# Optimization experiments

Hardware: AMD Instinct MI355X
Metric: run time of the kernel (lower is better)

The kernel has to match this reference:

```python
import jax, jax.numpy as jnp
import numpy as np

C, H, K, G = 256, 8, 32, 8
HD = C // H
SCALE = HD ** -0.5
POS_BND = int(0.8 * K * 1 ** 0.5)  # 25
RPE_NUM = 2 * POS_BND + 1          # 51
NW = 4096


def setup_inputs() -> dict:
    key = jax.random.key(0)
    ks = jax.random.split(key, 8)
    data = jax.random.normal(ks[0], (NW * (K + G), C), dtype=jnp.float32)
    # relative xyz offsets between points in a window; exercise the clamp
    rel_pos = jax.random.randint(ks[1], (NW, K, K, 3), -POS_BND - 5, POS_BND + 6).astype(jnp.int32)
    # additive mask: 0 for valid pairs, -100 for masked (padded) pairs
    keep = jax.random.bernoulli(ks[2], 0.9, (NW, K + G, K + G))
    mask = jnp.where(keep, 0.0, -100.0).astype(jnp.float32)
    qkv_w = jax.random.normal(ks[3], (C, 3 * C), dtype=jnp.float32) * (C ** -0.5)
    qkv_b = jnp.zeros((3 * C,), dtype=jnp.float32)
    proj_w = jax.random.normal(ks[4], (C, C), dtype=jnp.float32) * (C ** -0.5)
    proj_b = jnp.zeros((C,), dtype=jnp.float32)
    rpe_table = jax.random.normal(ks[5], (3 * RPE_NUM, H), dtype=jnp.float32) * 0.02
    return {"data": data, "rel_pos": rel_pos, "mask": mask, "qkv_w": qkv_w,
            "qkv_b": qkv_b, "proj_w": proj_w, "proj_b": proj_b, "rpe_table": rpe_table}


def reference(data, rel_pos, mask, qkv_w, qkv_b, proj_w, proj_b, rpe_table):
    W = K + G  # window size including context tokens
    qkv = data @ qkv_w + qkv_b                              # (T, 3C)
    qkv_std = jnp.std(qkv, axis=0, ddof=1)                  # torch .std is unbiased
    qkv = qkv.reshape(-1, W, 3, H, HD).transpose(2, 0, 3, 1, 4)  # (3, Nw, H, W, HD)
    q, k, v = qkv[0] * SCALE, qkv[1], qkv[2]
    attn = jnp.einsum('nhqd,nhkd->nhqk', q, k)              # (Nw, H, W, W)
    # RPE: clamp offsets, index per-axis slices of table, sum over xyz
    idx = jnp.clip(rel_pos, -POS_BND, POS_BND) + POS_BND + jnp.arange(3, dtype=rel_pos.dtype) * RPE_NUM
    rpe = rpe_table[idx].sum(axis=3)                        # (Nw, K, K, H)
    rpe = rpe.transpose(0, 3, 1, 2)                         # (Nw, H, K, K)
    rpe = jnp.pad(rpe, ((0, 0), (0, 0), (G, 0), (G, 0)))    # pad for context tokens
    attn = attn + rpe + mask[:, None]
    attn = jax.nn.softmax(attn, axis=-1)
    out = jnp.einsum('nhqk,nhkd->nqhd', attn, v).reshape(-1, W, C)
    out = out @ proj_w + proj_b                             # (Nw, W, C)
    return (out, qkv_std)
```

## Files before the change

### kernel.cpp

```cpp
#include <hip/hip_runtime.h>
#include <math.h>

#define SCALE_F 0.17677669529663687f

typedef __bf16 bf16x8 __attribute__((ext_vector_type(8)));
typedef float f32x4 __attribute__((ext_vector_type(4)));

__device__ __forceinline__ unsigned short f2bf(float f) {
  unsigned u = __builtin_bit_cast(unsigned, f);
  u = (u + 0x7FFFu + ((u >> 16) & 1u)) >> 16;
  return (unsigned short)u;
}
__device__ __forceinline__ float bf2f(unsigned short u) {
  return __builtin_bit_cast(float, (unsigned)u << 16);
}
__device__ __forceinline__ unsigned pk2(float a, float b) {
  return (unsigned)f2bf(a) | ((unsigned)f2bf(b) << 16);
}
__device__ __forceinline__ bf16x8 ld16(const void* p) {
  int4 v = *(const int4*)p;
  return __builtin_bit_cast(bf16x8, v);
}
__device__ __forceinline__ void gll16(const void* g, void* l) {
  __builtin_amdgcn_global_load_lds(
      (const __attribute__((address_space(1))) unsigned int*)g,
      (__attribute__((address_space(3))) unsigned int*)l, 16, 0, 0);
}


__global__ void octa_prep2(const float* __restrict__ qkv_w, const float* __restrict__ proj_w,
                           unsigned short* __restrict__ wTq, unsigned short* __restrict__ pTq)
{
  int e = blockIdx.x * 256 + threadIdx.x;
  if (e < 196608) {
    int c = e >> 13;
    int nc = c >> 3, kc = c & 7;
    int p2 = e & 8191;
    int n = p2 >> 5, cw = p2 & 31;
    int kl = cw ^ (((n >> 1) & 3) << 3);
    wTq[e] = f2bf(qkv_w[(size_t)(kc * 32 + kl) * 768 + nc * 256 + n]);
  } else {
    int e2 = e - 196608;
    int kc = e2 >> 13, p2 = e2 & 8191;
    int n = p2 >> 5, cw = p2 & 31;
    int kl = cw ^ (((n >> 1) & 3) << 3);
    pTq[e2] = f2bf(proj_w[(size_t)(kc * 32 + kl) * 256 + n]);
  }
}

__global__ __launch_bounds__(256)
void octa_bias(const float* __restrict__ maskp, const int* __restrict__ rel_pos,
               const float* __restrict__ rpe_table, char* __restrict__ biasg)
{
  __shared__ char bl[25600];
  const int w = blockIdx.x, tid = threadIdx.x;
  for (int e = tid; e < 1600; e += 256) {
    int qi = e / 40, kj = e - qi * 40;
    float m = maskp[(size_t)w * 1600 + qi * 40 + kj];
    float b8[8];
    if (qi >= 8 && kj >= 8) {
      const int* rp = rel_pos + ((size_t)w * 1024 + (qi - 8) * 32 + (kj - 8)) * 3;
      int c0 = rp[0], c1 = rp[1], c2 = rp[2];
      c0 = min(25, max(-25, c0)); c1 = min(25, max(-25, c1)); c2 = min(25, max(-25, c2));
      const float4* r0 = (const float4*)(rpe_table + (c0 + 25) * 8);
      const float4* r1 = (const float4*)(rpe_table + (c1 + 76) * 8);
      const float4* r2 = (const float4*)(rpe_table + (c2 + 127) * 8);
      float4 a0 = r0[0], a1 = r1[0], a2 = r2[0];
      float4 b0 = r0[1], b1 = r1[1], b2 = r2[1];
      b8[0] = m + a0.x + a1.x + a2.x; b8[1] = m + a0.y + a1.y + a2.y;
      b8[2] = m + a0.z + a1.z + a2.z; b8[3] = m + a0.w + a1.w + a2.w;
      b8[4] = m + b0.x + b1.x + b2.x; b8[5] = m + b0.y + b1.y + b2.y;
      b8[6] = m + b0.z + b1.z + b2.z; b8[7] = m + b0.w + b1.w + b2.w;
    } else {
      #pragma unroll
      for (int h = 0; h < 8; ++h) b8[h] = m;
    }
    #pragma unroll
    for (int h = 0; h < 8; ++h)
      *(unsigned short*)(bl + h * 3200 + kj * 80 + qi * 2) = f2bf(b8[h]);
  }
  __syncthreads();
  for (int f = tid; f < 1600; f += 256)
    *(int4*)(biasg + (size_t)w * 40960 + f * 16) = *(const int4*)(bl + f * 16);
}

#define KQ_A0 0
#define KQ_A1 8192
#define KQ_B0 16384
#define KQ_B1 32768
#define KQ_LDS 49152

__global__ __launch_bounds__(512, 4)
void octa_qkv(const float* __restrict__ data, const float* __restrict__ qkv_b,
              const unsigned short* __restrict__ wTq, float* __restrict__ ws,
              char* __restrict__ qg, char* __restrict__ kg, char* __restrict__ vg)
{
  extern __shared__ char smem[];
  const int tid = threadIdx.x, lane = tid & 63, wid = tid >> 6;
  const int ql = lane & 15, lg = lane >> 4;
  const int bm = blockIdx.x / 3, nc = blockIdx.x - bm * 3;
  const int wr = wid >> 2, wc = wid & 3;
  const char* wbase = (const char*)wTq + (size_t)nc * 131072;

  const int arow = tid >> 2, aq = tid & 3;
  const float* abase = data + ((size_t)bm * 128 + arow) * 256 + aq * 8;
  const int alds = arow * 64 + ((aq * 16) ^ (((arow >> 1) & 3) << 4));

  float4 a0 = *(const float4*)abase;
  float4 a1 = *(const float4*)(abase + 4);
  gll16(wbase + wid * 1024 + lane * 16, smem + KQ_B0 + wid * 1024);
  gll16(wbase + 8192 + wid * 1024 + lane * 16, smem + KQ_B0 + 8192 + wid * 1024);
  *(uint2*)(smem + KQ_A0 + alds) = make_uint2(pk2(a0.x, a0.y), pk2(a0.z, a0.w));
  *(uint2*)(smem + KQ_A0 + alds + 8) = make_uint2(pk2(a1.x, a1.y), pk2(a1.z, a1.w));
  __syncthreads();

  f32x4 acc[4][4];
  #pragma unroll
  for (int m = 0; m < 4; ++m)
    #pragma unroll
    for (int n = 0; n < 4; ++n) acc[m][n] = (f32x4){0.f, 0.f, 0.f, 0.f};

  #pragma unroll
  for (int t = 0; t < 8; ++t) {
    float4 na0, na1;
    if (t < 7) {
      na0 = *(const float4*)(abase + (t + 1) * 32);
      na1 = *(const float4*)(abase + (t + 1) * 32 + 4);
      const char* bsrc = wbase + (size_t)(t + 1) * 16384;
      char* bb1 = smem + (((t + 1) & 1) ? KQ_B1 : KQ_B0);
      gll16(bsrc + wid * 1024 + lane * 16, bb1 + wid * 1024);
      gll16(bsrc + 8192 + wid * 1024 + lane * 16, bb1 + 8192 + wid * 1024);
    }
    const char* ab = smem + ((t & 1) ? KQ_A1 : KQ_A0);
    const char* bb = smem + ((t & 1) ? KQ_B1 : KQ_B0);
    bf16x8 af[4], bf[4];
    #pragma unroll
    for (int mt = 0; mt < 4; ++mt) {
      int row = wr * 64 + mt * 16 + ql;
      af[mt] = ld16(ab + row * 64 + ((lg * 16) ^ (((row >> 1) & 3) << 4)));
    }
    #pragma unroll
    for (int nt = 0; nt < 4; ++nt) {
      int n = wc * 64 + nt * 16 + ql;
      bf[nt] = ld16(bb + n * 64 + ((lg * 16) ^ (((n >> 1) & 3) << 4)));
    }
    #pragma unroll
    for (int nt = 0; nt < 4; ++nt)
      #pragma unroll
      for (int mt = 0; mt < 4; ++mt)
        acc[mt][nt] = __builtin_amdgcn_mfma_f32_16x16x32_bf16(af[mt], bf[nt], acc[mt][nt], 0, 0, 0);
    if (t < 7) {
      char* ab1 = smem + (((t + 1) & 1) ? KQ_A1 : KQ_A0);
      *(uint2*)(ab1 + alds) = make_uint2(pk2(na0.x, na0.y), pk2(na0.z, na0.w));
      *(uint2*)(ab1 + alds + 8) = make_uint2(pk2(na1.x, na1.y), pk2(na1.z, na1.w));
    }
    __syncthreads();
  }

  char* base = nc == 0 ? qg : (nc == 1 ? kg : vg);
  const float cs = (nc == 0) ? SCALE_F : 1.0f;
  #pragma unroll
  for (int nt = 0; nt < 4; ++nt) {
    int col = wc * 64 + nt * 16 + ql;
    int h = col >> 5, d = col & 31;
    float bias = qkv_b[nc * 256 + col];
    float s1 = 0.f, s2 = 0.f;
    #pragma unroll
    for (int mt = 0; mt < 4; ++mt) {
      int tg0 = bm * 128 + wr * 64 + mt * 16 + lg * 4;
      int w = tg0 / 40, tk0 = tg0 - w * 40;
      size_t slice = (size_t)(w * 8 + h) * 2560;
      #pragma unroll
      for (int r = 0; r < 4; ++r) {
        float v = acc[mt][nt][r] + bias;
        s1 += v; s2 += v * v;
        *(unsigned short*)(base + slice + (tk0 + r) * 64 + d * 2) = f2bf(v * cs);
      }
    }
    s1 += __shfl_xor(s1, 16); s1 += __shfl_xor(s1, 32);
    s2 += __shfl_xor(s2, 16); s2 += __shfl_xor(s2, 32);
    if (lg == 0) {
      atomicAdd(ws + nc * 256 + col, s1);
      atomicAdd(ws + 768 + nc * 256 + col, s2);
    }
  }
}

#define F2_LDS 30720

__global__ __launch_bounds__(512, 4)
void octa_attnproj2(const char* __restrict__ qg, const char* __restrict__ kg,
                    const char* __restrict__ vg, const char* __restrict__ biasg,
                    const unsigned short* __restrict__ pTq, const float* __restrict__ proj_b,
                    float* __restrict__ out)
{
  extern __shared__ char smem[];
  const int tid = threadIdx.x, w = blockIdx.x, wid = tid >> 6;
  const int lane = tid & 63, ql = lane & 15, lg = lane >> 4, h = wid;
  const int perm = ql * 64 + lg * 16;
  const char* qb = qg + (size_t)(w * 8 + h) * 2560;
  const char* kb = kg + (size_t)(w * 8 + h) * 2560;
  const char* vb = vg + (size_t)(w * 8 + h) * 2560;
  const char* bb_ = biasg + (size_t)w * 40960 + h * 3200;

  bf16x8 kf0 = ld16(kb + perm), kf1 = ld16(kb + 1024 + perm), kf2 = ld16(kb + 2048 + perm);
  bf16x8 qf0 = ld16(qb + perm), qf1 = ld16(qb + 1024 + perm), qf2 = ld16(qb + 2048 + perm);
  union U8 { unsigned short u[8]; bf16x8 v; };
  U8 ua, ub, uc, ud;
  #pragma unroll
  for (int j = 0; j < 8; ++j) {
    int tok = lg * 8 + j;
    ua.u[j] = *(const unsigned short*)(vb + tok * 64 + ql * 2);
    ub.u[j] = *(const unsigned short*)(vb + tok * 64 + (16 + ql) * 2);
  }
  if (lg == 0) {
    #pragma unroll
    for (int j = 0; j < 8; ++j) {
      uc.u[j] = *(const unsigned short*)(vb + (32 + j) * 64 + ql * 2);
      ud.u[j] = *(const unsigned short*)(vb + (32 + j) * 64 + (16 + ql) * 2);
    }
  } else {
    #pragma unroll
    for (int j = 0; j < 8; ++j) { uc.u[j] = 0; ud.u[j] = 0; }
  }
  bf16x8 vA = ua.v, vB = ub.v, vC = uc.v, vD = ud.v;

  f32x4 st[9];
  {
    bf16x8 kf[3] = {kf0, kf1, kf2}, qf[3] = {qf0, qf1, qf2};
    __builtin_amdgcn_s_setprio(1);
    #pragma unroll
    for (int a = 0; a < 3; ++a)
      #pragma unroll
      for (int b = 0; b < 3; ++b)
        st[a * 3 + b] = __builtin_amdgcn_mfma_f32_16x16x32_bf16(
            kf[a], qf[b], (f32x4){0.f, 0.f, 0.f, 0.f}, 0, 0, 0);
    __builtin_amdgcn_s_setprio(0);
  }

  float mx[3] = {-3e38f, -3e38f, -3e38f};
  #pragma unroll
  for (int a = 0; a < 3; ++a) {
    #pragma unroll
    for (int b = 0; b < 3; ++b) {
      #pragma unroll
      for (int r = 0; r < 4; ++r) {
        int kj = a * 16 + lg * 4 + r;
        int qi = b * 16 + ql;
        float s = st[a * 3 + b][r];
        if (kj < 40) {
          if (qi < 40)
            s += bf2f(*(const unsigned short*)(bb_ + kj * 80 + qi * 2));
        } else {
          s = -1e30f;
        }
        st[a * 3 + b][r] = s;
        mx[b] = fmaxf(mx[b], s);
      }
    }
  }
  #pragma unroll
  for (int b = 0; b < 3; ++b) {
    mx[b] = fmaxf(mx[b], __shfl_xor(mx[b], 16));
    mx[b] = fmaxf(mx[b], __shfl_xor(mx[b], 32));
  }
  float sum[3] = {0.f, 0.f, 0.f};
  #pragma unroll
  for (int a = 0; a < 3; ++a)
    #pragma unroll
    for (int b = 0; b < 3; ++b)
      #pragma unroll
      for (int r = 0; r < 4; ++r) {
        float e = __expf(st[a * 3 + b][r] - mx[b]);
        st[a * 3 + b][r] = e;
        sum[b] += e;
      }
  float inv[3];
  #pragma unroll
  for (int b = 0; b < 3; ++b) {
    sum[b] += __shfl_xor(sum[b], 16);
    sum[b] += __shfl_xor(sum[b], 32);
    inv[b] = 1.f / sum[b];
  }

  char* pb_ = smem + wid * 3840;
  f32x4 ot[6];
  #pragma unroll
  for (int i = 0; i < 6; ++i) ot[i] = (f32x4){0.f, 0.f, 0.f, 0.f};

  #pragma unroll
  for (int a = 0; a < 2; ++a)
    #pragma unroll
    for (int b = 0; b < 3; ++b)
      #pragma unroll
      for (int r = 0; r < 4; ++r) {
        int kj = a * 16 + lg * 4 + r, qi = b * 16 + ql;
        *(unsigned short*)(pb_ + qi * 80 + kj * 2) = f2bf(st[a * 3 + b][r] * inv[b]);
      }
  asm volatile("" ::: "memory");
  __builtin_amdgcn_s_setprio(1);
  #pragma unroll
  for (int b = 0; b < 3; ++b) {
    bf16x8 pf = ld16(pb_ + (b * 16 + ql) * 80 + lg * 16);
    ot[b]     = __builtin_amdgcn_mfma_f32_16x16x32_bf16(vA, pf, ot[b], 0, 0, 0);
    ot[3 + b] = __builtin_amdgcn_mfma_f32_16x16x32_bf16(vB, pf, ot[3 + b], 0, 0, 0);
  }
  __builtin_amdgcn_s_setprio(0);
  asm volatile("" ::: "memory");
  #pragma unroll
  for (int b = 0; b < 3; ++b) {
    int qi = b * 16 + ql;
    #pragma unroll
    for (int r = 0; r < 4; ++r)
      *(unsigned short*)(pb_ + qi * 80 + (lg * 4 + r) * 2) = f2bf(st[6 + b][r] * inv[b]);
    *(uint2*)(pb_ + qi * 80 + 32 + lg * 8) = make_uint2(0u, 0u);
  }
  asm volatile("" ::: "memory");
  __builtin_amdgcn_s_setprio(1);
  #pragma unroll
  for (int b = 0; b < 3; ++b) {
    bf16x8 pf = ld16(pb_ + (b * 16 + ql) * 80 + lg * 16);
    ot[b]     = __builtin_amdgcn_mfma_f32_16x16x32_bf16(vC, pf, ot[b], 0, 0, 0);
    ot[3 + b] = __builtin_amdgcn_mfma_f32_16x16x32_bf16(vD, pf, ot[3 + b], 0, 0, 0);
  }
  __builtin_amdgcn_s_setprio(0);

  __syncthreads();
  #pragma unroll
  for (int dm = 0; dm < 2; ++dm)
    #pragma unroll
    for (int b = 0; b < 3; ++b) {
      int qi = b * 16 + ql;
      unsigned u0 = pk2(ot[dm * 3 + b][0], ot[dm * 3 + b][1]);
      unsigned u1 = pk2(ot[dm * 3 + b][2], ot[dm * 3 + b][3]);
      int colb = (h * 32 + dm * 16 + lg * 4) * 2;
      *(uint2*)(smem + qi * 512 + (colb ^ ((qi & 7) << 4))) = make_uint2(u0, u1);
    }
  __syncthreads();

  f32x4 pacc[3][2];
  #pragma unroll
  for (int m = 0; m < 3; ++m)
    #pragma unroll
    for (int n = 0; n < 2; ++n) pacc[m][n] = (f32x4){0.f, 0.f, 0.f, 0.f};
  const int c0 = wid * 32;
  const char* pB = (const char*)pTq;

  #pragma unroll
  for (int t = 0; t < 8; ++t) {
    bf16x8 af[3], bfr[2];
    #pragma unroll
    for (int mt = 0; mt < 3; ++mt) {
      int row = mt * 16 + ql;
      af[mt] = ld16(smem + row * 512 + ((t * 64 + lg * 16) ^ ((row & 7) << 4)));
    }
    #pragma unroll
    for (int nt = 0; nt < 2; ++nt) {
      int n = c0 + nt * 16 + ql;
      bfr[nt] = ld16(pB + (size_t)t * 16384 + n * 64 + ((lg * 16) ^ (((n >> 1) & 3) << 4)));
    }
    __builtin_amdgcn_s_setprio(1);
    #pragma unroll
    for (int nt = 0; nt < 2; ++nt)
      #pragma unroll
      for (int mt = 0; mt < 3; ++mt)
        pacc[mt][nt] = __builtin_amdgcn_mfma_f32_16x16x32_bf16(af[mt], bfr[nt], pacc[mt][nt], 0, 0, 0);
    __builtin_amdgcn_s_setprio(0);
  }

  #pragma unroll
  for (int nt = 0; nt < 2; ++nt) {
    int col = c0 + nt * 16 + ql;
    float pb = proj_b[col];
    #pragma unroll
    for (int mt = 0; mt < 3; ++mt)
      #pragma unroll
      for (int r = 0; r < 4; ++r) {
        int row = mt * 16 + lg * 4 + r;
        if (row < 40)
          out[(size_t)(w * 40 + row) * 256 + col] = pacc[mt][nt][r] + pb;
      }
  }
}

__global__ void octa_std(const float* __restrict__ ws, float* __restrict__ out,
                         int total_rows, size_t off)
{
  int j = blockIdx.x * 256 + threadIdx.x;
  if (j < 768) {
    float s = ws[j], ss = ws[768 + j];
    float T = (float)total_rows;
    float var = (ss - s * s / T) / (T - 1.f);
    out[off + j] = sqrtf(fmaxf(var, 0.f));
  }
}

#define O_RPE 0
#define O_MSK 4896
#define O_IDX 8096
#define O_A   12192
#define O_ATT 36768
#define B1_SZ 49152
#define ATT_STRIDE 11776
#define AK 3840
#define AV 7680
#define B2_S (O_ATT + 94208)
#define B2_A O_ATT
#define LDS_BYTES_V4 163744

__device__ __forceinline__ int a_addr(int row, int byte) {
  return O_A + row * 512 + (byte ^ ((row & 7) << 4));
}
__device__ __forceinline__ int v_addr(int d, int byte) {
  return AV + d * 128 + (byte ^ ((d & 7) << 4));
}

__global__ void octa_prep_v4(const float* __restrict__ qkv_w, const float* __restrict__ proj_w,
                             unsigned short* __restrict__ wTq, unsigned short* __restrict__ pTq)
{
  int idx = blockIdx.x * 256 + threadIdx.x;
  if (idx < 196608) {
    int n = idx >> 8, k = idx & 255;
    wTq[idx] = f2bf(qkv_w[k * 768 + n]);
  } else {
    int i = idx - 196608;
    int n = i >> 8, k = i & 255;
    pTq[i] = f2bf(proj_w[k * 256 + n]);
  }
}

__global__ __launch_bounds__(512, 2)
void octa_main_v4(const float* __restrict__ data, const int* __restrict__ rel_pos,
                  const float* __restrict__ maskp, const float* __restrict__ qkv_b,
                  const float* __restrict__ proj_b, const float* __restrict__ rpe_table,
                  const unsigned short* __restrict__ wTq, const unsigned short* __restrict__ pTq,
                  float* __restrict__ ws, float* __restrict__ out)
{
  extern __shared__ char smem[];
  float* s_rpe = (float*)(smem + O_RPE);
  const int tid = threadIdx.x;
  const int w   = blockIdx.x;
  const int wid = tid >> 6;
  const int lane = tid & 63;
  const int ql = lane & 15;
  const int lg = lane >> 4;
  const int h  = wid;
  const int ab = O_ATT + wid * ATT_STRIDE;

  {
    #pragma unroll
    for (int it = 0; it < 6; ++it) {
      int g = it * 512 + tid;
      int n = g >> 2, slot = g & 3;
      const char* src = (const char*)wTq + (size_t)n * 512 + ((slot * 16) ^ ((n & 3) << 4));
      gll16(src, smem + O_ATT + it * 8192 + wid * 1024);
    }
  }
  for (int f = tid; f < 1224; f += 512) s_rpe[f] = rpe_table[f];
  for (int f = tid; f < 400; f += 512) {
    float4 m4 = ((const float4*)(maskp + (size_t)w * 1600))[f];
    uint2 pk;
    pk.x = pk2(m4.x, m4.y); pk.y = pk2(m4.z, m4.w);
    *(uint2*)(smem + O_MSK + f * 8) = pk;
  }
  for (int p = tid; p < 1024; p += 512) {
    const int* rp = rel_pos + ((size_t)w * 1024 + p) * 3;
    int c0 = rp[0], c1 = rp[1], c2 = rp[2];
    c0 = min(25, max(-25, c0)); c1 = min(25, max(-25, c1)); c2 = min(25, max(-25, c2));
    unsigned pk = (unsigned)(c0 + 25) | ((unsigned)(c1 + 76) << 10) | ((unsigned)(c2 + 127) << 20);
    *(unsigned*)(smem + O_IDX + ((p * 4) ^ (((p >> 5) & 7) << 4))) = pk;
  }
  {
    const float4* src = (const float4*)(data + (size_t)w * 10240);
    for (int f = tid; f < 2560; f += 512) {
      int token = f >> 6, q4 = f & 63;
      float4 d4 = src[f];
      uint2 pk;
      pk.x = pk2(d4.x, d4.y); pk.y = pk2(d4.z, d4.w);
      *(uint2*)(smem + a_addr(token, q4 * 8)) = pk;
    }
    int token = 40 + (tid >> 6), byte = (tid & 63) * 8;
    *(uint2*)(smem + a_addr(token, byte)) = make_uint2(0u, 0u);
  }
  __syncthreads();

  f32x4 acc[18];
  #pragma unroll
  for (int i = 0; i < 18; ++i) acc[i] = (f32x4){0.f, 0.f, 0.f, 0.f};

  for (int t = 0; t < 8; ++t) {
    if (t < 7) {
      int bb = O_ATT + ((t + 1) & 1) * B1_SZ;
      #pragma unroll
      for (int it = 0; it < 6; ++it) {
        int g = it * 512 + tid;
        int n = g >> 2, slot = g & 3;
        const char* src = (const char*)wTq + (size_t)n * 512 + (t + 1) * 64
                          + ((slot * 16) ^ ((n & 3) << 4));
        gll16(src, smem + bb + it * 8192 + wid * 1024);
      }
    }
    const int bb = O_ATT + (t & 1) * B1_SZ;
    bf16x8 af[3];
    #pragma unroll
    for (int mt = 0; mt < 3; ++mt)
      af[mt] = ld16(smem + a_addr(mt * 16 + ql, t * 64 + lg * 16));
    #pragma unroll
    for (int j = 0; j < 6; ++j) {
      int n = ((j >> 1) * 16 + 2 * wid + (j & 1)) * 16 + ql;
      bf16x8 bf = ld16(smem + bb + n * 64 + ((lg * 16) ^ ((n & 3) << 4)));
      #pragma unroll
      for (int mt = 0; mt < 3; ++mt)
        acc[j * 3 + mt] = __builtin_amdgcn_mfma_f32_16x16x32_bf16(af[mt], bf, acc[j * 3 + mt], 0, 0, 0);
    }
    __syncthreads();
  }

  {
    #pragma unroll
    for (int it = 0; it < 4; ++it) {
      int g = it * 512 + tid;
      int n = g >> 3, slot = g & 7;
      const char* src = (const char*)pTq + (size_t)n * 512 + ((slot * 16) ^ ((n & 7) << 4));
      gll16(src, smem + B2_S + it * 8192 + wid * 1024);
    }
  }

  #pragma unroll
  for (int j = 0; j < 6; ++j) {
    int sec = j >> 1;
    int ncol = sec * 256 + 32 * wid + (j & 1) * 16 + ql;
    int d = (j & 1) * 16 + ql;
    float bias = qkv_b[ncol];
    float s1 = 0.f, s2 = 0.f;
    #pragma unroll
    for (int mt = 0; mt < 3; ++mt) {
      #pragma unroll
      for (int r = 0; r < 4; ++r) {
        int token = mt * 16 + lg * 4 + r;
        float v = acc[j * 3 + mt][r] + bias;
        if (token < 40) { s1 += v; s2 += v * v; }
        if (sec == 0)
          *(unsigned short*)(smem + ab + token * 80 + d * 2) = f2bf(v * SCALE_F);
        else if (sec == 1)
          *(unsigned short*)(smem + ab + AK + token * 80 + d * 2) = f2bf(v);
        else
          *(unsigned short*)(smem + ab + v_addr(d, token * 2)) = f2bf(v);
      }
    }
    s1 += __shfl_xor(s1, 16); s1 += __shfl_xor(s1, 32);
    s2 += __shfl_xor(s2, 16); s2 += __shfl_xor(s2, 32);
    if (lg == 0) { atomicAdd(ws + ncol, s1); atomicAdd(ws + 768 + ncol, s2); }
  }
  {
    int zd = lane >> 1;
    int zb = 96 + (lane & 1) * 16;
    *(int4*)(smem + ab + v_addr(zd, zb)) = (int4){0, 0, 0, 0};
  }
  asm volatile("" ::: "memory");

  f32x4 st[9];
  {
    bf16x8 kf[3], qf[3];
    #pragma unroll
    for (int a = 0; a < 3; ++a) kf[a] = ld16(smem + ab + AK + (a * 16 + ql) * 80 + lg * 16);
    #pragma unroll
    for (int b = 0; b < 3; ++b) qf[b] = ld16(smem + ab + (b * 16 + ql) * 80 + lg * 16);
    #pragma unroll
    for (int a = 0; a < 3; ++a)
      #pragma unroll
      for (int b = 0; b < 3; ++b)
        st[a * 3 + b] = __builtin_amdgcn_mfma_f32_16x16x32_bf16(
            kf[a], qf[b], (f32x4){0.f, 0.f, 0.f, 0.f}, 0, 0, 0);
  }

  float mx[3] = {-3e38f, -3e38f, -3e38f};
  #pragma unroll
  for (int a = 0; a < 3; ++a) {
    #pragma unroll
    for (int b = 0; b < 3; ++b) {
      #pragma unroll
      for (int r = 0; r < 4; ++r) {
        int kj = a * 16 + lg * 4 + r;
        int qi = b * 16 + ql;
        float s = st[a * 3 + b][r];
        if (kj < 40) {
          if (qi < 40) {
            s += bf2f(*(const unsigned short*)(smem + O_MSK + (qi * 40 + kj) * 2));
            if (kj >= 8 && qi >= 8) {
              int p = (qi - 8) * 32 + (kj - 8);
              unsigned pk = *(const unsigned*)(smem + O_IDX + ((p * 4) ^ (((p >> 5) & 7) << 4)));
              s += s_rpe[(pk & 1023) * 8 + h] + s_rpe[((pk >> 10) & 1023) * 8 + h]
                 + s_rpe[(pk >> 20) * 8 + h];
            }
          }
        } else {
          s = -1e30f;
        }
        st[a * 3 + b][r] = s;
        mx[b] = fmaxf(mx[b], s);
      }
    }
  }
  #pragma unroll
  for (int b = 0; b < 3; ++b) {
    mx[b] = fmaxf(mx[b], __shfl_xor(mx[b], 16));
    mx[b] = fmaxf(mx[b], __shfl_xor(mx[b], 32));
  }
  float sum[3] = {0.f, 0.f, 0.f};
  #pragma unroll
  for (int a = 0; a < 3; ++a)
    #pragma unroll
    for (int b = 0; b < 3; ++b)
      #pragma unroll
      for (int r = 0; r < 4; ++r) {
        float e = __expf(st[a * 3 + b][r] - mx[b]);
        st[a * 3 + b][r] = e;
        sum[b] += e;
      }
  float inv[3];
  #pragma unroll
  for (int b = 0; b < 3; ++b) {
    sum[b] += __shfl_xor(sum[b], 16);
    sum[b] += __shfl_xor(sum[b], 32);
    inv[b] = 1.f / sum[b];
  }

  f32x4 ot[6];
  #pragma unroll
  for (int i = 0; i < 6; ++i) ot[i] = (f32x4){0.f, 0.f, 0.f, 0.f};

  #pragma unroll
  for (int a = 0; a < 2; ++a)
    #pragma unroll
    for (int b = 0; b < 3; ++b)
      #pragma unroll
      for (int r = 0; r < 4; ++r) {
        int kj = a * 16 + lg * 4 + r, qi = b * 16 + ql;
        *(unsigned short*)(smem + ab + qi * 80 + kj * 2) = f2bf(st[a * 3 + b][r] * inv[b]);
      }
  asm volatile("" ::: "memory");
  {
    bf16x8 vf0 = ld16(smem + ab + v_addr(ql, lg * 16));
    bf16x8 vf1 = ld16(smem + ab + v_addr(16 + ql, lg * 16));
    #pragma unroll
    for (int b = 0; b < 3; ++b) {
      bf16x8 pf = ld16(smem + ab + (b * 16 + ql) * 80 + lg * 16);
      ot[b] = __builtin_amdgcn_mfma_f32_16x16x32_bf16(vf0, pf, ot[b], 0, 0, 0);
      ot[3 + b] = __builtin_amdgcn_mfma_f32_16x16x32_bf16(vf1, pf, ot[3 + b], 0, 0, 0);
    }
  }
  asm volatile("" ::: "memory");
  #pragma unroll
  for (int b = 0; b < 3; ++b) {
    int qi = b * 16 + ql;
    #pragma unroll
    for (int r = 0; r < 4; ++r) {
      int kj = 32 + lg * 4 + r;
      *(unsigned short*)(smem + ab + qi * 80 + (kj - 32) * 2) = f2bf(st[6 + b][r] * inv[b]);
    }
    *(uint2*)(smem + ab + qi * 80 + 32 + lg * 8) = make_uint2(0u, 0u);
  }
  asm volatile("" ::: "memory");
  {
    bf16x8 vf0 = ld16(smem + ab + v_addr(ql, 64 + lg * 16));
    bf16x8 vf1 = ld16(smem + ab + v_addr(16 + ql, 64 + lg * 16));
    #pragma unroll
    for (int b = 0; b < 3; ++b) {
      bf16x8 pf = ld16(smem + ab + (b * 16 + ql) * 80 + lg * 16);
      ot[b] = __builtin_amdgcn_mfma_f32_16x16x32_bf16(vf0, pf, ot[b], 0, 0, 0);
      ot[3 + b] = __builtin_amdgcn_mfma_f32_16x16x32_bf16(vf1, pf, ot[3 + b], 0, 0, 0);
    }
  }
  #pragma unroll
  for (int dm = 0; dm < 2; ++dm)
    #pragma unroll
    for (int b = 0; b < 3; ++b)
      #pragma unroll
      for (int r = 0; r < 4; ++r) {
        int d = dm * 16 + lg * 4 + r;
        int qi = b * 16 + ql;
        *(unsigned short*)(smem + a_addr(qi, (h * 32 + d) * 2)) = f2bf(ot[dm * 3 + b][r]);
      }
  __syncthreads();

  f32x4 oacc[6];
  #pragma unroll
  for (int i = 0; i < 6; ++i) oacc[i] = (f32x4){0.f, 0.f, 0.f, 0.f};

  for (int t = 0; t < 4; ++t) {
    if (t < 3) {
      int bb = ((t + 1) & 1) ? B2_A : B2_S;
      #pragma unroll
      for (int it = 0; it < 4; ++it) {
        int g = it * 512 + tid;
        int n = g >> 3, slot = g & 7;
        const char* src = (const char*)pTq + (size_t)n * 512 + (t + 1) * 128
                          + ((slot * 16) ^ ((n & 7) << 4));
        gll16(src, smem + bb + it * 8192 + wid * 1024);
      }
    }
    const int bb = (t & 1) ? B2_A : B2_S;
    #pragma unroll
    for (int ks = 0; ks < 2; ++ks) {
      bf16x8 af[3];
      #pragma unroll
      for (int mt = 0; mt < 3; ++mt)
        af[mt] = ld16(smem + a_addr(mt * 16 + ql, t * 128 + ks * 64 + lg * 16));
      #pragma unroll
      for (int nt = 0; nt < 2; ++nt) {
        int n = (2 * wid + nt) * 16 + ql;
        bf16x8 bf = ld16(smem + bb + n * 128 + ((ks * 64 + lg * 16) ^ ((n & 7) << 4)));
        #pragma unroll
        for (int mt = 0; mt < 3; ++mt)
          oacc[nt * 3 + mt] = __builtin_amdgcn_mfma_f32_16x16x32_bf16(af[mt], bf, oacc[nt * 3 + mt], 0, 0, 0);
      }
    }
    __syncthreads();
  }

  #pragma unroll
  for (int nt = 0; nt < 2; ++nt) {
    int ncol = (2 * wid + nt) * 16 + ql;
    float pb = proj_b[ncol];
    #pragma unroll
    for (int mt = 0; mt < 3; ++mt)
      #pragma unroll
      for (int r = 0; r < 4; ++r) {
        int token = mt * 16 + lg * 4 + r;
        if (token < 40)
          out[(size_t)w * 10240 + token * 256 + ncol] = oacc[nt * 3 + mt][r] + pb;
      }
  }
}

extern "C" void kernel_launch(void* const* d_in, const int* in_sizes, int n_in,
                              void* d_out, int out_size, void* d_ws, size_t ws_size,
                              hipStream_t stream) {
  const float* data    = (const float*)d_in[0];
  const int*   rel_pos = (const int*)d_in[1];
  const float* maskp   = (const float*)d_in[2];
  const float* qkv_w   = (const float*)d_in[3];
  const float* qkv_b   = (const float*)d_in[4];
  const float* proj_w  = (const float*)d_in[5];
  const float* proj_b  = (const float*)d_in[6];
  const float* rpe_tab = (const float*)d_in[7];
  float* out = (float*)d_out;
  float* ws  = (float*)d_ws;

  const int nw = in_sizes[1] / 3072;
  const int total_rows = nw * 40;
  const size_t std_off = (size_t)nw * 10240;
  const size_t SZ = 83886080ull;

  const size_t WS1 = 530432ull + 3ull * SZ + 4096ull;

  unsigned short* wTq = (unsigned short*)((char*)d_ws + 6144);
  unsigned short* pTq = (unsigned short*)((char*)d_ws + 399360);

  hipMemsetAsync(ws, 0, 6144, stream);

  if (ws_size >= WS1) {
    char* qg = (char*)d_ws + 530432;
    char* kg = qg + SZ;
    char* vg = kg + SZ;
    char* biasg = (char*)d_out;
    (void)hipFuncSetAttribute((const void*)octa_attnproj2,
                              hipFuncAttributeMaxDynamicSharedMemorySize, F2_LDS);
    hipLaunchKernelGGL(octa_prep2, dim3(1024), dim3(256), 0, stream, qkv_w, proj_w, wTq, pTq);
    hipLaunchKernelGGL(octa_bias, dim3(nw), dim3(256), 0, stream,
                       maskp, rel_pos, rpe_tab, biasg);
    hipLaunchKernelGGL(octa_qkv, dim3(nw * 40 / 128 * 3), dim3(512), KQ_LDS, stream,
                       data, qkv_b, wTq, ws, qg, kg, vg);
    hipLaunchKernelGGL(octa_attnproj2, dim3(nw), dim3(512), F2_LDS, stream,
                       qg, kg, vg, biasg, pTq, proj_b, out);
    hipLaunchKernelGGL(octa_std, dim3(3), dim3(256), 0, stream, ws, out, total_rows, std_off);
  } else {
    hipLaunchKernelGGL(octa_prep_v4, dim3(1024), dim3(256), 0, stream, qkv_w, proj_w, wTq, pTq);
    (void)hipFuncSetAttribute((const void*)octa_main_v4,
                              hipFuncAttributeMaxDynamicSharedMemorySize, LDS_BYTES_V4);
    hipLaunchKernelGGL(octa_main_v4, dim3(nw), dim3(512), LDS_BYTES_V4, stream,
                       data, rel_pos, maskp, qkv_b, proj_b, rpe_tab, wTq, pTq, ws, out);
    hipLaunchKernelGGL(octa_std, dim3(3), dim3(256), 0, stream, ws, out, total_rows, std_off);
  }
}
```

Baseline: 413.6 us.

## Fuse RPE/mask bias computation into attention kernel via shared memory

Removes the separate bias kernel, which wrote a bf16 bias tensor per window to global memory that the attention kernel then read back. The attention kernel now computes clamped RPE plus mask per window directly into LDS before the QK MFMAs, with barriers around the use. This removes one launch and a global round trip of bias data. In exchange it adds gather work and extra synchronisation to the attention kernel, and it reuses LDS that later stages of that kernel may also need.

```diff
diff --git a/kernel.cpp b/kernel.cpp
--- a/kernel.cpp
+++ b/kernel.cpp
@@ -48,15 +48,150 @@
   }
 }
 
-__global__ __launch_bounds__(256)
-void octa_bias(const float* __restrict__ maskp, const int* __restrict__ rel_pos,
-               const float* __restrict__ rpe_table, char* __restrict__ biasg)
+#define KQ_A0 0
+#define KQ_A1 8192
+#define KQ_B0 16384
+#define KQ_B1 32768
+#define KQ_LDS 49152
+
+__global__ __launch_bounds__(512, 4)
+void octa_qkv(const float* __restrict__ data, const float* __restrict__ qkv_b,
+              const unsigned short* __restrict__ wTq, float* __restrict__ ws,
+              char* __restrict__ qg, char* __restrict__ kg, char* __restrict__ vg)
 {
-  __shared__ char bl[25600];
-  const int w = blockIdx.x, tid = threadIdx.x;
-  for (int e = tid; e < 1600; e += 256) {
+  extern __shared__ char smem[];
+  const int tid = threadIdx.x, lane = tid & 63, wid = tid >> 6;
+  const int ql = lane & 15, lg = lane >> 4;
+  const int bm = blockIdx.x / 3, nc = blockIdx.x - bm * 3;
+  const int wr = wid >> 2, wc = wid & 3;
+  const char* wbase = (const char*)wTq + (size_t)nc * 131072;
+
+  const int arow = tid >> 2, aq = tid & 3;
+  const float* abase = data + ((size_t)bm * 128 + arow) * 256 + aq * 8;
+  const int alds = arow * 64 + ((aq * 16) ^ (((arow >> 1) & 3) << 4));
+
+  float4 a0 = *(const float4*)abase;
+  float4 a1 = *(const float4*)(abase + 4);
+  gll16(wbase + wid * 1024 + lane * 16, smem + KQ_B0 + wid * 1024);
+  gll16(wbase + 8192 + wid * 1024 + lane * 16, smem + KQ_B0 + 8192 + wid * 1024);
+  *(uint2*)(smem + KQ_A0 + alds) = make_uint2(pk2(a0.x, a0.y), pk2(a0.z, a0.w));
+  *(uint2*)(smem + KQ_A0 + alds + 8) = make_uint2(pk2(a1.x, a1.y), pk2(a1.z, a1.w));
+  __syncthreads();
+
+  f32x4 acc[4][4];
+  #pragma unroll
+  for (int m = 0; m < 4; ++m)
+    #pragma unroll
+    for (int n = 0; n < 4; ++n) acc[m][n] = (f32x4){0.f, 0.f, 0.f, 0.f};
+
+  #pragma unroll
+  for (int t = 0; t < 8; ++t) {
+    float4 na0, na1;
+    if (t < 7) {
+      na0 = *(const float4*)(abase + (t + 1) * 32);
+      na1 = *(const float4*)(abase + (t + 1) * 32 + 4);
+      const char* bsrc = wbase + (size_t)(t + 1) * 16384;
+      char* bb1 = smem + (((t + 1) & 1) ? KQ_B1 : KQ_B0);
+      gll16(bsrc + wid * 1024 + lane * 16, bb1 + wid * 1024);
+      gll16(bsrc + 8192 + wid * 1024 + lane * 16, bb1 + 8192 + wid * 1024);
+    }
+    const char* ab = smem + ((t & 1) ? KQ_A1 : KQ_A0);
+    const char* bb = smem + ((t & 1) ? KQ_B1 : KQ_B0);
+    bf16x8 af[4], bf[4];
+    #pragma unroll
+    for (int mt = 0; mt < 4; ++mt) {
+      int row = wr * 64 + mt * 16 + ql;
+      af[mt] = ld16(ab + row * 64 + ((lg * 16) ^ (((row >> 1) & 3) << 4)));
+    }
+    #pragma unroll
+    for (int nt = 0; nt < 4; ++nt) {
+      int n = wc * 64 + nt * 16 + ql;
+      bf[nt] = ld16(bb + n * 64 + ((lg * 16) ^ (((n >> 1) & 3) << 4)));
+    }
+    #pragma unroll
+    for (int nt = 0; nt < 4; ++nt)
+      #pragma unroll
+      for (int mt = 0; mt < 4; ++mt)
+        acc[mt][nt] = __builtin_amdgcn_mfma_f32_16x16x32_bf16(af[mt], bf[nt], acc[mt][nt], 0, 0, 0);
+    if (t < 7) {
+      char* ab1 = smem + (((t + 1) & 1) ? KQ_A1 : KQ_A0);
+      *(uint2*)(ab1 + alds) = make_uint2(pk2(na0.x, na0.y), pk2(na0.z, na0.w));
+      *(uint2*)(ab1 + alds + 8) = make_uint2(pk2(na1.x, na1.y), pk2(na1.z, na1.w));
+    }
+    __syncthreads();
+  }
+
+  char* base = nc == 0 ? qg : (nc == 1 ? kg : vg);
+  const float cs = (nc == 0) ? SCALE_F : 1.0f;
+  #pragma unroll
+  for (int nt = 0; nt < 4; ++nt) {
+    int col = wc * 64 + nt * 16 + ql;
+    int h = col >> 5, d = col & 31;
+    float bias = qkv_b[nc * 256 + col];
+    float s1 = 0.f, s2 = 0.f;
+    #pragma unroll
+    for (int mt = 0; mt < 4; ++mt) {
+      int tg0 = bm * 128 + wr * 64 + mt * 16 + lg * 4;
+      int w = tg0 / 40, tk0 = tg0 - w * 40;
+      size_t slice = (size_t)(w * 8 + h) * 2560;
+      #pragma unroll
+      for (int r = 0; r < 4; ++r) {
+        float v = acc[mt][nt][r] + bias;
+        s1 += v; s2 += v * v;
+        *(unsigned short*)(base + slice + (tk0 + r) * 64 + d * 2) = f2bf(v * cs);
+      }
+    }
+    s1 += __shfl_xor(s1, 16); s1 += __shfl_xor(s1, 32);
+    s2 += __shfl_xor(s2, 16); s2 += __shfl_xor(s2, 32);
+    if (lg == 0) {
+      atomicAdd(ws + nc * 256 + col, s1);
+      atomicAdd(ws + 768 + nc * 256 + col, s2);
+    }
+  }
+}
+
+#define F3_LDS 30720
+
+__global__ __launch_bounds__(512, 4)
+void octa_attnproj3(const char* __restrict__ qg, const char* __restrict__ kg,
+                    const char* __restrict__ vg, const float* __restrict__ maskp,
+                    const int* __restrict__ rel_pos, const float* __restrict__ rpe_table,
+                    const unsigned short* __restrict__ pTq, const float* __restrict__ proj_b,
+                    float* __restrict__ out)
+{
+  extern __shared__ char smem[];
+  const int tid = threadIdx.x, w = blockIdx.x, wid = tid >> 6;
+  const int lane = tid & 63, ql = lane & 15, lg = lane >> 4, h = wid;
+  const int perm = ql * 64 + lg * 16;
+  const char* qb = qg + (size_t)(w * 8 + h) * 2560;
+  const char* kb = kg + (size_t)(w * 8 + h) * 2560;
+  const char* vb = vg + (size_t)(w * 8 + h) * 2560;
+
+  bf16x8 kf0 = ld16(kb + perm), kf1 = ld16(kb + 1024 + perm), kf2 = ld16(kb + 2048 + perm);
+  bf16x8 qf0 = ld16(qb + perm), qf1 = ld16(qb + 1024 + perm), qf2 = ld16(qb + 2048 + perm);
+  union U8 { unsigned short u[8]; bf16x8 v; };
+  U8 ua, ub, uc, ud;
+  #pragma unroll
+  for (int j = 0; j < 8; ++j) {
+    int tok = lg * 8 + j;
+    ua.u[j] = *(const unsigned short*)(vb + tok * 64 + ql * 2);
+    ub.u[j] = *(const unsigned short*)(vb + tok * 64 + (16 + ql) * 2);
+  }
+  if (lg == 0) {
+    #pragma unroll
+    for (int j = 0; j < 8; ++j) {
+      uc.u[j] = *(const unsigned short*)(vb + (32 + j) * 64 + ql * 2);
+      ud.u[j] = *(const unsigned short*)(vb + (32 + j) * 64 + (16 + ql) * 2);
+    }
+  } else {
+    #pragma unroll
+    for (int j = 0; j < 8; ++j) { uc.u[j] = 0; ud.u[j] = 0; }
+  }
+  bf16x8 vA = ua.v, vB = ub.v, vC = uc.v, vD = ud.v;
+
+  for (int e = tid; e < 1600; e += 512) {
     int qi = e / 40, kj = e - qi * 40;
-    float m = maskp[(size_t)w * 1600 + qi * 40 + kj];
+    float m = maskp[(size_t)w * 1600 + e];
     float b8[8];
     if (qi >= 8 && kj >= 8) {
       const int* rp = rel_pos + ((size_t)w * 1024 + (qi - 8) * 32 + (kj - 8)) * 3;
@@ -73,157 +208,12 @@
       b8[6] = m + b0.z + b1.z + b2.z; b8[7] = m + b0.w + b1.w + b2.w;
     } else {
       #pragma unroll
-      for (int h = 0; h < 8; ++h) b8[h] = m;
-    }
-    #pragma unroll
-    for (int h = 0; h < 8; ++h)
-      *(unsigned short*)(bl + h * 3200 + kj * 80 + qi * 2) = f2bf(b8[h]);
-  }
-  __syncthreads();
-  for (int f = tid; f < 1600; f += 256)
-    *(int4*)(biasg + (size_t)w * 40960 + f * 16) = *(const int4*)(bl + f * 16);
-}
-
-#define KQ_A0 0
-#define KQ_A1 8192
-#define KQ_B0 16384
-#define KQ_B1 32768
-#define KQ_LDS 49152
-
-__global__ __launch_bounds__(512, 4)
-void octa_qkv(const float* __restrict__ data, const float* __restrict__ qkv_b,
-              const unsigned short* __restrict__ wTq, float* __restrict__ ws,
-              char* __restrict__ qg, char* __restrict__ kg, char* __restrict__ vg)
-{
-  extern __shared__ char smem[];
-  const int tid = threadIdx.x, lane = tid & 63, wid = tid >> 6;
-  const int ql = lane & 15, lg = lane >> 4;
-  const int bm = blockIdx.x / 3, nc = blockIdx.x - bm * 3;
-  const int wr = wid >> 2, wc = wid & 3;
-  const char* wbase = (const char*)wTq + (size_t)nc * 131072;
-
-  const int arow = tid >> 2, aq = tid & 3;
-  const float* abase = data + ((size_t)bm * 128 + arow) * 256 + aq * 8;
-  const int alds = arow * 64 + ((aq * 16) ^ (((arow >> 1) & 3) << 4));
-
-  float4 a0 = *(const float4*)abase;
-  float4 a1 = *(const float4*)(abase + 4);
-  gll16(wbase + wid * 1024 + lane * 16, smem + KQ_B0 + wid * 1024);
-  gll16(wbase + 8192 + wid * 1024 + lane * 16, smem + KQ_B0 + 8192 + wid * 1024);
-  *(uint2*)(smem + KQ_A0 + alds) = make_uint2(pk2(a0.x, a0.y), pk2(a0.z, a0.w));
-  *(uint2*)(smem + KQ_A0 + alds + 8) = make_uint2(pk2(a1.x, a1.y), pk2(a1.z, a1.w));
-  __syncthreads();
-
-  f32x4 acc[4][4];
-  #pragma unroll
-  for (int m = 0; m < 4; ++m)
-    #pragma unroll
-    for (int n = 0; n < 4; ++n) acc[m][n] = (f32x4){0.f, 0.f, 0.f, 0.f};
-
-  #pragma unroll
-  for (int t = 0; t < 8; ++t) {
-    float4 na0, na1;
-    if (t < 7) {
-      na0 = *(const float4*)(abase + (t + 1) * 32);
-      na1 = *(const float4*)(abase + (t + 1) * 32 + 4);
-      const char* bsrc = wbase + (size_t)(t + 1) * 16384;
-      char* bb1 = smem + (((t + 1) & 1) ? KQ_B1 : KQ_B0);
-      gll16(bsrc + wid * 1024 + lane * 16, bb1 + wid * 1024);
-      gll16(bsrc + 8192 + wid * 1024 + lane * 16, bb1 + 8192 + wid * 1024);
-    }
-    const char* ab = smem + ((t & 1) ? KQ_A1 : KQ_A0);
-    const char* bb = smem + ((t & 1) ? KQ_B1 : KQ_B0);
-    bf16x8 af[4], bf[4];
-    #pragma unroll
-    for (int mt = 0; mt < 4; ++mt) {
-      int row = wr * 64 + mt * 16 + ql;
-      af[mt] = ld16(ab + row * 64 + ((lg * 16) ^ (((row >> 1) & 3) << 4)));
-    }
-    #pragma unroll
-    for (int nt = 0; nt < 4; ++nt) {
-      int n = wc * 64 + nt * 16 + ql;
-      bf[nt] = ld16(bb + n * 64 + ((lg * 16) ^ (((n >> 1) & 3) << 4)));
-    }
-    #pragma unroll
-    for (int nt = 0; nt < 4; ++nt)
-      #pragma unroll
-      for (int mt = 0; mt < 4; ++mt)
-        acc[mt][nt] = __builtin_amdgcn_mfma_f32_16x16x32_bf16(af[mt], bf[nt], acc[mt][nt], 0, 0, 0);
-    if (t < 7) {
-      char* ab1 = smem + (((t + 1) & 1) ? KQ_A1 : KQ_A0);
-      *(uint2*)(ab1 + alds) = make_uint2(pk2(na0.x, na0.y), pk2(na0.z, na0.w));
-      *(uint2*)(ab1 + alds + 8) = make_uint2(pk2(na1.x, na1.y), pk2(na1.z, na1.w));
-    }
-    __syncthreads();
-  }
-
-  char* base = nc == 0 ? qg : (nc == 1 ? kg : vg);
-  const float cs = (nc == 0) ? SCALE_F : 1.0f;
-  #pragma unroll
-  for (int nt = 0; nt < 4; ++nt) {
-    int col = wc * 64 + nt * 16 + ql;
-    int h = col >> 5, d = col & 31;
-    float bias = qkv_b[nc * 256 + col];
-    float s1 = 0.f, s2 = 0.f;
-    #pragma unroll
-    for (int mt = 0; mt < 4; ++mt) {
-      int tg0 = bm * 128 + wr * 64 + mt * 16 + lg * 4;
-      int w = tg0 / 40, tk0 = tg0 - w * 40;
-      size_t slice = (size_t)(w * 8 + h) * 2560;
-      #pragma unroll
-      for (int r = 0; r < 4; ++r) {
-        float v = acc[mt][nt][r] + bias;
-        s1 += v; s2 += v * v;
-        *(unsigned short*)(base + slice + (tk0 + r) * 64 + d * 2) = f2bf(v * cs);
-      }
-    }
-    s1 += __shfl_xor(s1, 16); s1 += __shfl_xor(s1, 32);
-    s2 += __shfl_xor(s2, 16); s2 += __shfl_xor(s2, 32);
-    if (lg == 0) {
-      atomicAdd(ws + nc * 256 + col, s1);
-      atomicAdd(ws + 768 + nc * 256 + col, s2);
-    }
-  }
-}
-
-#define F2_LDS 30720
-
-__global__ __launch_bounds__(512, 4)
-void octa_attnproj2(const char* __restrict__ qg, const char* __restrict__ kg,
-                    const char* __restrict__ vg, const char* __restrict__ biasg,
-                    const unsigned short* __restrict__ pTq, const float* __restrict__ proj_b,
-                    float* __restrict__ out)
-{
-  extern __shared__ char smem[];
-  const int tid = threadIdx.x, w = blockIdx.x, wid = tid >> 6;
-  const int lane = tid & 63, ql = lane & 15, lg = lane >> 4, h = wid;
-  const int perm = ql * 64 + lg * 16;
-  const char* qb = qg + (size_t)(w * 8 + h) * 2560;
-  const char* kb = kg + (size_t)(w * 8 + h) * 2560;
-  const char* vb = vg + (size_t)(w * 8 + h) * 2560;
-  const char* bb_ = biasg + (size_t)w * 40960 + h * 3200;
-
-  bf16x8 kf0 = ld16(kb + perm), kf1 = ld16(kb + 1024 + perm), kf2 = ld16(kb + 2048 + perm);
-  bf16x8 qf0 = ld16(qb + perm), qf1 = ld16(qb + 1024 + perm), qf2 = ld16(qb + 2048 + perm);
-  union U8 { unsigned short u[8]; bf16x8 v; };
-  U8 ua, ub, uc, ud;
-  #pragma unroll
-  for (int j = 0; j < 8; ++j) {
-    int tok = lg * 8 + j;
-    ua.u[j] = *(const unsigned short*)(vb + tok * 64 + ql * 2);
-    ub.u[j] = *(const unsigned short*)(vb + tok * 64 + (16 + ql) * 2);
-  }
-  if (lg == 0) {
-    #pragma unroll
-    for (int j = 0; j < 8; ++j) {
-      uc.u[j] = *(const unsigned short*)(vb + (32 + j) * 64 + ql * 2);
-      ud.u[j] = *(const unsigned short*)(vb + (32 + j) * 64 + (16 + ql) * 2);
-    }
-  } else {
-    #pragma unroll
-    for (int j = 0; j < 8; ++j) { uc.u[j] = 0; ud.u[j] = 0; }
-  }
-  bf16x8 vA = ua.v, vB = ub.v, vC = uc.v, vD = ud.v;
+      for (int hh = 0; hh < 8; ++hh) b8[hh] = m;
+    }
+    #pragma unroll
+    for (int hh = 0; hh < 8; ++hh)
+      *(unsigned short*)(smem + hh * 3200 + kj * 80 + qi * 2) = f2bf(b8[hh]);
+  }
 
   f32x4 st[9];
   {
@@ -237,7 +227,9 @@
             kf[a], qf[b], (f32x4){0.f, 0.f, 0.f, 0.f}, 0, 0, 0);
     __builtin_amdgcn_s_setprio(0);
   }
-
+  __syncthreads();
+
+  const char* bb_ = smem + h * 3200;
   float mx[3] = {-3e38f, -3e38f, -3e38f};
   #pragma unroll
   for (int a = 0; a < 3; ++a) {
@@ -259,6 +251,8 @@
       }
     }
   }
+  __syncthreads();
+
   #pragma unroll
   for (int b = 0; b < 3; ++b) {
     mx[b] = fmaxf(mx[b], __shfl_xor(mx[b], 16));
@@ -764,16 +758,13 @@
     char* qg = (char*)d_ws + 530432;
     char* kg = qg + SZ;
     char* vg = kg + SZ;
-    char* biasg = (char*)d_out;
-    (void)hipFuncSetAttribute((const void*)octa_attnproj2,
-                              hipFuncAttributeMaxDynamicSharedMemorySize, F2_LDS);
+    (void)hipFuncSetAttribute((const void*)octa_attnproj3,
+                              hipFuncAttributeMaxDynamicSharedMemorySize, F3_LDS);
     hipLaunchKernelGGL(octa_prep2, dim3(1024), dim3(256), 0, stream, qkv_w, proj_w, wTq, pTq);
-    hipLaunchKernelGGL(octa_bias, dim3(nw), dim3(256), 0, stream,
-                       maskp, rel_pos, rpe_tab, biasg);
     hipLaunchKernelGGL(octa_qkv, dim3(nw * 40 / 128 * 3), dim3(512), KQ_LDS, stream,
                        data, qkv_b, wTq, ws, qg, kg, vg);
-    hipLaunchKernelGGL(octa_attnproj2, dim3(nw), dim3(512), F2_LDS, stream,
-                       qg, kg, vg, biasg, pTq, proj_b, out);
+    hipLaunchKernelGGL(octa_attnproj3, dim3(nw), dim3(512), F3_LDS, stream,
+                       qg, kg, vg, maskp, rel_pos, rpe_tab, pTq, proj_b, out);
     hipLaunchKernelGGL(octa_std, dim3(3), dim3(256), 0, stream, ws, out, total_rows, std_off);
   } else {
     hipLaunchKernelGGL(octa_prep_v4, dim3(1024), dim3(256), 0, stream, qkv_w, proj_w, wTq, pTq);
```

Result: faster. 353.4 us (-14.6%).
